# Performance work log

Measured on AMD Instinct MI355X. Metric: run time of the kernel, lower is better.

## Reference

```python
import jax, jax.numpy as jnp
import numpy as np

N_HEAD = 16
E = 1024
B, T = 2, 2048


def setup_inputs() -> dict:
    key = jax.random.key(0)
    ks = jax.random.split(key, 5)
    s = 1.0 / np.sqrt(E)
    return {
        "x": jax.random.normal(ks[0], (B, T, E), dtype=jnp.float32),
        "w_qkv": jax.random.normal(ks[1], (E, 3 * E), dtype=jnp.float32) * s,
        "b_qkv": jnp.zeros((3 * E,), dtype=jnp.float32),
        "w_proj": jax.random.normal(ks[2], (E, E), dtype=jnp.float32) * s,
        "b_proj": jnp.zeros((E,), dtype=jnp.float32),
    }


def reference(x, w_qkv, b_qkv, w_proj, b_proj):
    Bsz, Tlen, Emb = x.shape
    hd = Emb // N_HEAD
    qkv = x @ w_qkv + b_qkv  # [B, T, 3E]
    q, k, v = jnp.split(qkv, 3, axis=-1)
    # [B, H, T, hd]
    q = q.reshape(Bsz, Tlen, N_HEAD, hd).transpose(0, 2, 1, 3)
    k = k.reshape(Bsz, Tlen, N_HEAD, hd).transpose(0, 2, 1, 3)
    v = v.reshape(Bsz, Tlen, N_HEAD, hd).transpose(0, 2, 1, 3)
    scale = 1.0 / jnp.sqrt(jnp.asarray(hd, dtype=x.dtype))
    scores = jnp.einsum("bhqd,bhkd->bhqk", q, k) * scale  # [B, H, T, T]
    causal = jnp.tril(jnp.ones((Tlen, Tlen), dtype=bool))
    scores = jnp.where(causal, scores, jnp.asarray(-jnp.inf, dtype=scores.dtype))
    attn = jax.nn.softmax(scores, axis=-1)
    y = jnp.einsum("bhqk,bhkd->bhqd", attn, v)  # [B, H, T, hd]
    y = y.transpose(0, 2, 1, 3).reshape(Bsz, Tlen, Emb)
    return y @ w_proj + b_proj
```

## Files before the change

kernel.cpp:

```cpp
#include <hip/hip_runtime.h>
#include <hip/hip_bf16.h>

typedef __hip_bfloat16 bf16;
typedef __attribute__((ext_vector_type(8))) short sh8;
typedef __attribute__((ext_vector_type(4))) float f32x4;

#define BB 2
#define TT 2048
#define EE 1024
#define NH 16
#define HD 64
#define M_ROWS (BB * TT)
#define PPAD 72

__device__ __forceinline__ float b2f(bf16 v) { return __bfloat162float(v); }
__device__ __forceinline__ bf16 f2b(float v) { return __float2bfloat16(v); }
__device__ __forceinline__ unsigned short f2bu(float v) {
    union { bf16 b; unsigned short u; } x; x.b = f2b(v); return x.u;
}

__device__ __forceinline__ void gl2lds16(const bf16* g, bf16* l) {
    __builtin_amdgcn_global_load_lds(
        (__attribute__((address_space(1))) void*)g,
        (__attribute__((address_space(3))) void*)l, 16, 0, 0);
}

__global__ __launch_bounds__(256) void prep(
    const float* __restrict__ x, bf16* __restrict__ xb,
    const float* __restrict__ Wq, bf16* __restrict__ Wqt,
    const float* __restrict__ Wp, bf16* __restrict__ Wpt) {
    const int bid = blockIdx.x;
    if (bid < 4096) {
        const int i = bid * 256 + threadIdx.x;
        const float4 v = ((const float4*)x)[i];
        ushort4 u;
        u.x = f2bu(v.x); u.y = f2bu(v.y); u.z = f2bu(v.z); u.w = f2bu(v.w);
        ((ushort4*)xb)[i] = u;
        return;
    }
    __shared__ float Ld[64][65];
    const float* src; bf16* dst; int ncols, nc0, kr0;
    if (bid < 4096 + 768) {
        const int t = bid - 4096;
        src = Wq; dst = Wqt; ncols = 3072;
        nc0 = (t % 48) * 64; kr0 = (t / 48) * 64;
    } else {
        const int t = bid - 4096 - 768;
        src = Wp; dst = Wpt; ncols = 1024;
        nc0 = (t % 16) * 64; kr0 = (t / 16) * 64;
    }
#pragma unroll
    for (int i = 0; i < 16; ++i) {
        const int e = threadIdx.x + i * 256;
        Ld[e >> 6][e & 63] = src[(size_t)(kr0 + (e >> 6)) * ncols + nc0 + (e & 63)];
    }
    __syncthreads();
#pragma unroll
    for (int i = 0; i < 16; ++i) {
        const int e = threadIdx.x + i * 256;
        const int r2 = e & 63, c2 = e >> 6;
        dst[(size_t)(nc0 + c2) * EE + kr0 + r2] = f2b(Ld[r2][c2]);
    }
}

__device__ __forceinline__ void mfma_gemm_core(
    const bf16* __restrict__ A, const bf16* __restrict__ Bt,
    int m0, int n0, f32x4 acc[4][4], bf16* Al, bf16* Bl) {
    const int tid = threadIdx.x, w = tid >> 6, lane = tid & 63;
    const int li = lane & 15, quad = lane >> 4;
    const int wm = (w & 1) * 64, wn = (w >> 1) * 64;
    const int srow = w * 32 + (lane >> 3);
    const int scol = (lane & 7) * 8;

#pragma unroll
    for (int mt = 0; mt < 4; ++mt)
#pragma unroll
        for (int nt = 0; nt < 4; ++nt) acc[mt][nt] = (f32x4){0.f, 0.f, 0.f, 0.f};

    for (int k0 = 0; k0 < EE; k0 += 64) {
        __syncthreads();
#pragma unroll
        for (int j = 0; j < 4; ++j) {
            const int row = srow + j * 8;
            const int sk = scol ^ ((row & 7) * 8);
            gl2lds16(A  + (size_t)(m0 + row) * EE + k0 + sk, Al + row * 64 + scol);
            gl2lds16(Bt + (size_t)(n0 + row) * EE + k0 + sk, Bl + row * 64 + scol);
        }
        __syncthreads();
#pragma unroll
        for (int ks = 0; ks < 2; ++ks) {
            const int kof = (ks * 32 + quad * 8) ^ ((li & 7) * 8);
            sh8 af[4], bv[4];
#pragma unroll
            for (int mt = 0; mt < 4; ++mt)
                af[mt] = *(const sh8*)(Al + (wm + mt * 16 + li) * 64 + kof);
#pragma unroll
            for (int nt = 0; nt < 4; ++nt)
                bv[nt] = *(const sh8*)(Bl + (wn + nt * 16 + li) * 64 + kof);
#pragma unroll
            for (int mt = 0; mt < 4; ++mt)
#pragma unroll
                for (int nt = 0; nt < 4; ++nt)
                    acc[mt][nt] = __builtin_amdgcn_mfma_f32_16x16x32_bf16(
                        af[mt], bv[nt], acc[mt][nt], 0, 0, 0);
        }
    }
}

#define QBM 256
#define QBN 256
#define QBK 64
#define QNT (EE / QBK)

__global__ __launch_bounds__(512, 2) void gemm_qkv_8ph(
    const bf16* __restrict__ A, const bf16* __restrict__ Bt,
    const float* __restrict__ bias,
    bf16* __restrict__ Qb, bf16* __restrict__ Kb, bf16* __restrict__ Vb) {
    __shared__ bf16 Al[2][QBM * QBK];
    __shared__ bf16 Bl[2][QBN * QBK];

    const int tid  = threadIdx.x;
    const int lane = tid & 63;
    const int w    = tid >> 6;
    const int li   = lane & 15, quad = lane >> 4;
    const int wr   = w >> 2, wc = w & 3;
    const int wm   = wr << 7, wn = wc << 6;
    const int m0   = blockIdx.y << 8, n0 = blockIdx.x << 8;

    const int srow = tid >> 3;
    const int scol = (tid & 7) << 3;
    const int sg   = scol ^ ((srow & 7) << 3);
    const int swz  = (li & 7) << 3;
    const int kof0 = (quad << 3) ^ swz;
    const int kof1 = (32 + (quad << 3)) ^ swz;

    f32x4 acc[8][4];
#pragma unroll
    for (int m = 0; m < 8; ++m)
#pragma unroll
        for (int n = 0; n < 4; ++n) acc[m][n] = (f32x4){0.f, 0.f, 0.f, 0.f};

    sh8 ra[8][2];
    sh8 rb[4][2];

#define QSTAGE_A(t, h) do {                                                    \
        const int _k0 = (t) * QBK; bf16* _lb = &Al[(t) & 1][0];                \
        _Pragma("unroll")                                                      \
        for (int _j = 0; _j < 2; ++_j) {                                       \
            const int _r = ((h) << 7) + (_j << 6) + srow;                      \
            gl2lds16(A + (size_t)(m0 + _r) * EE + _k0 + sg,                    \
                     _lb + _r * QBK + scol);                                   \
        }                                                                      \
    } while (0)

#define QSTAGE_B(t, h) do {                                                    \
        const int _k0 = (t) * QBK; bf16* _lb = &Bl[(t) & 1][0];                \
        _Pragma("unroll")                                                      \
        for (int _j = 0; _j < 2; ++_j) {                                       \
            const int _r = ((h) << 7) + (_j << 6) + srow;                      \
            gl2lds16(Bt + (size_t)(n0 + _r) * EE + _k0 + sg,                   \
                     _lb + _r * QBK + scol);                                   \
        }                                                                      \
    } while (0)

#define QLOAD_A(cb, a) do {                                                    \
        const bf16* _ab = &Al[cb][0];                                          \
        _Pragma("unroll")                                                      \
        for (int _m = 0; _m < 4; ++_m) {                                       \
            const int _row = wm + (((a) << 2) + _m) * 16 + li;                 \
            ra[((a) << 2) + _m][0] = *(const sh8*)(_ab + _row * QBK + kof0);   \
            ra[((a) << 2) + _m][1] = *(const sh8*)(_ab + _row * QBK + kof1);   \
        }                                                                      \
    } while (0)

#define QLOAD_B(cb, b) do {                                                    \
        const bf16* _bb = &Bl[cb][0];                                          \
        _Pragma("unroll")                                                      \
        for (int _n = 0; _n < 2; ++_n) {                                       \
            const int _row = wn + (((b) << 1) + _n) * 16 + li;                 \
            rb[((b) << 1) + _n][0] = *(const sh8*)(_bb + _row * QBK + kof0);   \
            rb[((b) << 1) + _n][1] = *(const sh8*)(_bb + _row * QBK + kof1);   \
        }                                                                      \
    } while (0)

#define QMFMA(a, b) do {                                                       \
        _Pragma("unroll")                                                      \
        for (int _m = 0; _m < 4; ++_m)                                         \
            _Pragma("unroll")                                                  \
            for (int _n = 0; _n < 2; ++_n) {                                   \
                acc[((a) << 2) + _m][((b) << 1) + _n] =                        \
                    __builtin_amdgcn_mfma_f32_16x16x32_bf16(                   \
                        ra[((a) << 2) + _m][0], rb[((b) << 1) + _n][0],        \
                        acc[((a) << 2) + _m][((b) << 1) + _n], 0, 0, 0);       \
                acc[((a) << 2) + _m][((b) << 1) + _n] =                        \
                    __builtin_amdgcn_mfma_f32_16x16x32_bf16(                   \
                        ra[((a) << 2) + _m][1], rb[((b) << 1) + _n][1],        \
                        acc[((a) << 2) + _m][((b) << 1) + _n], 0, 0, 0);       \
            }                                                                  \
    } while (0)

#define PH_MID() do { __builtin_amdgcn_s_barrier();                            \
        asm volatile("s_waitcnt lgkmcnt(0)" ::: "memory");                     \
        __builtin_amdgcn_s_setprio(1); } while (0)
#define PH_END() do { __builtin_amdgcn_s_setprio(0);                           \
        __builtin_amdgcn_s_barrier(); } while (0)
#define PH_END_VM4() do { __builtin_amdgcn_s_setprio(0);                       \
        asm volatile("s_waitcnt vmcnt(4)" ::: "memory");                       \
        __builtin_amdgcn_s_barrier(); } while (0)

    QSTAGE_A(0, 0); QSTAGE_A(0, 1); QSTAGE_B(0, 0); QSTAGE_B(0, 1);
    QSTAGE_A(1, 0); QSTAGE_A(1, 1);
    asm volatile("s_waitcnt vmcnt(4)" ::: "memory");
    __builtin_amdgcn_s_barrier();

#pragma unroll 1
    for (int i = 0; i < QNT / 2 - 1; ++i) {
        const int t1 = 2 * i + 1, t2 = 2 * i + 2, t3 = 2 * i + 3;
        QLOAD_A(0, 0); QLOAD_B(0, 0); QSTAGE_B(t1, 0);
        PH_MID(); QMFMA(0, 0); PH_END();
        QLOAD_A(0, 1); QSTAGE_B(t1, 1);
        PH_MID(); QMFMA(1, 0); PH_END();
        QLOAD_B(0, 1); QSTAGE_A(t2, 0);
        PH_MID(); QMFMA(0, 1); PH_END();
        QSTAGE_A(t2, 1);
        PH_MID(); QMFMA(1, 1); PH_END_VM4();
        QLOAD_A(1, 0); QLOAD_B(1, 0); QSTAGE_B(t2, 0);
        PH_MID(); QMFMA(0, 0); PH_END();
        QLOAD_A(1, 1); QSTAGE_B(t2, 1);
        PH_MID(); QMFMA(1, 0); PH_END();
        QLOAD_B(1, 1); QSTAGE_A(t3, 0);
        PH_MID(); QMFMA(0, 1); PH_END();
        QSTAGE_A(t3, 1);
        PH_MID(); QMFMA(1, 1); PH_END_VM4();
    }

    QSTAGE_B(QNT - 1, 0); QSTAGE_B(QNT - 1, 1);
    QLOAD_A(0, 0); QLOAD_B(0, 0); QMFMA(0, 0);
    QLOAD_A(0, 1); QMFMA(1, 0);
    QLOAD_B(0, 1); QMFMA(0, 1); QMFMA(1, 1);
    asm volatile("s_waitcnt vmcnt(0)" ::: "memory");
    __builtin_amdgcn_s_barrier();
    QLOAD_A(1, 0); QLOAD_B(1, 0); QMFMA(0, 0);
    QLOAD_A(1, 1); QMFMA(1, 0);
    QLOAD_B(1, 1); QMFMA(0, 1); QMFMA(1, 1);

#undef QSTAGE_A
#undef QSTAGE_B
#undef QLOAD_A
#undef QLOAD_B
#undef QMFMA
#undef PH_MID
#undef PH_END
#undef PH_END_VM4

    const int which = n0 >> 10;
#pragma unroll
    for (int nt = 0; nt < 4; ++nt) {
        const int n = n0 + wn + nt * 16 + li;
        const int hseg = n & 1023;
        const int h = hseg >> 6, d = hseg & 63;
        const float bv = bias[n];
        if (which == 2) {
#pragma unroll
            for (int mt = 0; mt < 8; ++mt) {
                const int mb = m0 + wm + mt * 16 + quad * 4;
                const int b = mb >> 11, t = mb & (TT - 1);
                ushort4 u;
                u.x = f2bu(acc[mt][nt][0] + bv);
                u.y = f2bu(acc[mt][nt][1] + bv);
                u.z = f2bu(acc[mt][nt][2] + bv);
                u.w = f2bu(acc[mt][nt][3] + bv);
                *(ushort4*)(Vb + ((size_t)((b * NH + h) * HD + d)) * TT + t) = u;
            }
        } else {
            bf16* dst = (which == 0) ? Qb : Kb;
            const float scl = (which == 0) ? 0.125f : 1.0f;
#pragma unroll
            for (int mt = 0; mt < 8; ++mt)
#pragma unroll
                for (int r = 0; r < 4; ++r) {
                    const int m = m0 + wm + mt * 16 + quad * 4 + r;
                    const int b = m >> 11, t = m & (TT - 1);
                    dst[((size_t)(b * NH + h) * TT + t) * HD + d] =
                        f2b((acc[mt][nt][r] + bv) * scl);
                }
        }
    }
}

__global__ __launch_bounds__(256) void gemm_proj_mfma(
    const bf16* __restrict__ A, const bf16* __restrict__ Bt,
    const float* __restrict__ bias, float* __restrict__ C) {
    __shared__ bf16 Al[128 * 64];
    __shared__ bf16 Bl[128 * 64];
    f32x4 acc[4][4];
    const int m0 = blockIdx.y * 128, n0 = blockIdx.x * 128;
    mfma_gemm_core(A, Bt, m0, n0, acc, Al, Bl);

    const int tid = threadIdx.x, w = tid >> 6, lane = tid & 63;
    const int li = lane & 15, quad = lane >> 4;
    const int wm = (w & 1) * 64, wn = (w >> 1) * 64;

#pragma unroll
    for (int nt = 0; nt < 4; ++nt) {
        const int n = n0 + wn + nt * 16 + li;
        const float bv = bias[n];
#pragma unroll
        for (int mt = 0; mt < 4; ++mt)
#pragma unroll
            for (int r = 0; r < 4; ++r) {
                const int m = m0 + wm + mt * 16 + quad * 4 + r;
                C[(size_t)m * EE + n] = acc[mt][nt][r] + bv;
            }
    }
}

__global__ __launch_bounds__(256) void attn_mfma(
    const bf16* __restrict__ Q, const bf16* __restrict__ K,
    const bf16* __restrict__ Vt, bf16* __restrict__ Y) {
    __shared__ bf16 Kl[2][64 * 64];
    __shared__ bf16 Vl[2][64 * 64];
    __shared__ bf16 Pl[4][16 * PPAD];

    const int tid  = threadIdx.x;
    const int w    = tid >> 6;
    const int lane = tid & 63;
    const int li   = lane & 15;
    const int quad = lane >> 4;
    const int swz  = (li & 7) * 8;
    const int idx  = blockIdx.x;
    const int qb   = 31 - (idx >> 5);
    const int bh   = idx & 31;
    const int q0   = qb << 6;
    const int qw0  = q0 + w * 16;

    const bf16* Qb = Q  + (size_t)bh * TT * HD;
    const bf16* Kb = K  + (size_t)bh * TT * HD;
    const bf16* Vb = Vt + (size_t)bh * HD * TT;

    sh8 qf0 = *(const sh8*)(Qb + (size_t)(qw0 + li) * HD + quad * 8);
    sh8 qf1 = *(const sh8*)(Qb + (size_t)(qw0 + li) * HD + 32 + quad * 8);

    f32x4 o[4];
#pragma unroll
    for (int nt = 0; nt < 4; ++nt) o[nt] = (f32x4){0.f, 0.f, 0.f, 0.f};
    float lacc = 0.f;

    const int l8 = lane >> 3, l7 = lane & 7;
    const int gcol = ((l7 ^ l8) * 8);

    const int ntiles = qb + 1;
#pragma unroll
    for (int c = 0; c < 2; ++c) {
        const int rb = w * 16 + c * 8;
        gl2lds16(Kb + (size_t)(rb + l8) * HD + gcol, &Kl[0][rb * 64]);
        gl2lds16(Vb + (size_t)(rb + l8) * TT + gcol, &Vl[0][rb * 64]);
    }

    for (int it = 0; it < ntiles; ++it) {
        const int cur = it & 1;
        __syncthreads();
        if (it + 1 < ntiles) {
            const int j1 = (it + 1) << 6;
            const int nxt = cur ^ 1;
#pragma unroll
            for (int c = 0; c < 2; ++c) {
                const int rb = w * 16 + c * 8;
                gl2lds16(Kb + (size_t)(j1 + rb + l8) * HD + gcol, &Kl[nxt][rb * 64]);
                gl2lds16(Vb + (size_t)(rb + l8) * TT + j1 + gcol, &Vl[nxt][rb * 64]);
            }
        }
        const bf16* kb = &Kl[cur][0];
        const bf16* vb = &Vl[cur][0];

        const bool diag = (it == ntiles - 1);
#pragma unroll
        for (int nt = 0; nt < 4; ++nt) {
            f32x4 a = (f32x4){0.f, 0.f, 0.f, 0.f};
            sh8 kf0 = *(const sh8*)(kb + (nt * 16 + li) * 64 + ((quad * 8) ^ swz));
            a = __builtin_amdgcn_mfma_f32_16x16x32_bf16(kf0, qf0, a, 0, 0, 0);
            sh8 kf1 = *(const sh8*)(kb + (nt * 16 + li) * 64 + ((32 + quad * 8) ^ swz));
            a = __builtin_amdgcn_mfma_f32_16x16x32_bf16(kf1, qf1, a, 0, 0, 0);

            ushort4 u;
            float p0, p1, p2, p3;
            if (diag) {
                const int keyb = q0 + nt * 16 + quad * 4;
                const int qg = qw0 + li;
                p0 = (keyb + 0 > qg) ? 0.f : __expf(a[0]);
                p1 = (keyb + 1 > qg) ? 0.f : __expf(a[1]);
                p2 = (keyb + 2 > qg) ? 0.f : __expf(a[2]);
                p3 = (keyb + 3 > qg) ? 0.f : __expf(a[3]);
            } else {
                p0 = __expf(a[0]); p1 = __expf(a[1]);
                p2 = __expf(a[2]); p3 = __expf(a[3]);
            }
            lacc += (p0 + p1) + (p2 + p3);
            u.x = f2bu(p0); u.y = f2bu(p1); u.z = f2bu(p2); u.w = f2bu(p3);
            *(ushort4*)(&Pl[w][li * PPAD + nt * 16 + quad * 4]) = u;
        }

#pragma unroll
        for (int ks = 0; ks < 2; ++ks) {
            sh8 pf = *(const sh8*)(&Pl[w][li * PPAD + ks * 32 + quad * 8]);
#pragma unroll
            for (int nt = 0; nt < 4; ++nt) {
                sh8 vf = *(const sh8*)(vb + (nt * 16 + li) * 64 +
                                       ((ks * 32 + quad * 8) ^ swz));
                o[nt] = __builtin_amdgcn_mfma_f32_16x16x32_bf16(pf, vf, o[nt], 0, 0, 0);
            }
        }
    }

    lacc += __shfl_xor(lacc, 16, 64);
    lacc += __shfl_xor(lacc, 32, 64);
    float rinv[4];
#pragma unroll
    for (int r = 0; r < 4; ++r)
        rinv[r] = 1.0f / __shfl(lacc, quad * 4 + r, 64);

    const int b = bh >> 4, h = bh & 15;
#pragma unroll
    for (int nt = 0; nt < 4; ++nt)
#pragma unroll
        for (int r = 0; r < 4; ++r) {
            const int q = qw0 + quad * 4 + r;
            Y[((size_t)(b * TT + q)) * EE + h * HD + nt * 16 + li] =
                f2b(o[nt][r] * rinv[r]);
        }
}

extern "C" void kernel_launch(void* const* d_in, const int* in_sizes, int n_in,
                              void* d_out, int out_size, void* d_ws, size_t ws_size,
                              hipStream_t stream) {
    const float* x      = (const float*)d_in[0];
    const float* w_qkv  = (const float*)d_in[1];
    const float* b_qkv  = (const float*)d_in[2];
    const float* w_proj = (const float*)d_in[3];
    const float* b_proj = (const float*)d_in[4];
    float* out = (float*)d_out;

    const size_t SZ = (size_t)M_ROWS * EE;
    bf16* Q   = (bf16*)d_ws;
    bf16* K   = Q + SZ;
    bf16* V   = K + SZ;
    bf16* XB  = V + SZ;
    bf16* WQT = XB + SZ;
    bf16* WPT = WQT + 3 * SZ / 4;
    bf16* Y   = XB;

    prep<<<dim3(4096 + 768 + 256), dim3(256), 0, stream>>>(
        x, XB, w_qkv, WQT, w_proj, WPT);

    gemm_qkv_8ph<<<dim3(12, 16), dim3(512), 0, stream>>>(XB, WQT, b_qkv, Q, K, V);

    attn_mfma<<<dim3((TT / 64) * (BB * NH)), dim3(256), 0, stream>>>(Q, K, V, Y);

    gemm_proj_mfma<<<dim3(8, 32), dim3(256), 0, stream>>>(Y, WPT, b_proj, out);
}
```

Baseline: 184.5 us.

## Halve A-fragment registers by reordering MFMA quadrants in QKV GEMM pipeline

Reorders the four MFMA sub-tiles per K-step into a serpentine order (00, 01, 11, 10) so only four A fragments are live at once, and splits the B fragments into two double-buffered register sets. The global-to-LDS staging schedule is reshuffled to match, prefetching B ahead instead of A, and the epilogue is rewritten with phased barriers. The aim is to cut VGPR pressure in the 256x256-tile GEMM, which can free registers or allow better overlap. The more complex staging order risks LDS hazards or extra stalls.

```diff
diff --git a/kernel.cpp b/kernel.cpp
--- a/kernel.cpp
+++ b/kernel.cpp
@@ -140,8 +140,9 @@
 #pragma unroll
         for (int n = 0; n < 4; ++n) acc[m][n] = (f32x4){0.f, 0.f, 0.f, 0.f};
 
-    sh8 ra[8][2];
-    sh8 rb[4][2];
+    sh8 ra[4][2];
+    sh8 rb0[2][2];
+    sh8 rb1[2][2];
 
 #define QSTAGE_A(t, h) do {                                                    \
         const int _k0 = (t) * QBK; bf16* _lb = &Al[(t) & 1][0];                \
@@ -168,33 +169,33 @@
         _Pragma("unroll")                                                      \
         for (int _m = 0; _m < 4; ++_m) {                                       \
             const int _row = wm + (((a) << 2) + _m) * 16 + li;                 \
-            ra[((a) << 2) + _m][0] = *(const sh8*)(_ab + _row * QBK + kof0);   \
-            ra[((a) << 2) + _m][1] = *(const sh8*)(_ab + _row * QBK + kof1);   \
+            ra[_m][0] = *(const sh8*)(_ab + _row * QBK + kof0);                \
+            ra[_m][1] = *(const sh8*)(_ab + _row * QBK + kof1);                \
         }                                                                      \
     } while (0)
 
-#define QLOAD_B(cb, b) do {                                                    \
+#define QLOAD_B(cb, b, R) do {                                                 \
         const bf16* _bb = &Bl[cb][0];                                          \
         _Pragma("unroll")                                                      \
         for (int _n = 0; _n < 2; ++_n) {                                       \
             const int _row = wn + (((b) << 1) + _n) * 16 + li;                 \
-            rb[((b) << 1) + _n][0] = *(const sh8*)(_bb + _row * QBK + kof0);   \
-            rb[((b) << 1) + _n][1] = *(const sh8*)(_bb + _row * QBK + kof1);   \
+            R[_n][0] = *(const sh8*)(_bb + _row * QBK + kof0);                 \
+            R[_n][1] = *(const sh8*)(_bb + _row * QBK + kof1);                 \
         }                                                                      \
     } while (0)
 
-#define QMFMA(a, b) do {                                                       \
+#define QMFMA(a, b, R) do {                                                    \
         _Pragma("unroll")                                                      \
         for (int _m = 0; _m < 4; ++_m)                                         \
             _Pragma("unroll")                                                  \
             for (int _n = 0; _n < 2; ++_n) {                                   \
                 acc[((a) << 2) + _m][((b) << 1) + _n] =                        \
                     __builtin_amdgcn_mfma_f32_16x16x32_bf16(                   \
-                        ra[((a) << 2) + _m][0], rb[((b) << 1) + _n][0],        \
+                        ra[_m][0], R[_n][0],                                   \
                         acc[((a) << 2) + _m][((b) << 1) + _n], 0, 0, 0);       \
                 acc[((a) << 2) + _m][((b) << 1) + _n] =                        \
                     __builtin_amdgcn_mfma_f32_16x16x32_bf16(                   \
-                        ra[((a) << 2) + _m][1], rb[((b) << 1) + _n][1],        \
+                        ra[_m][1], R[_n][1],                                   \
                         acc[((a) << 2) + _m][((b) << 1) + _n], 0, 0, 0);       \
             }                                                                  \
     } while (0)
@@ -207,42 +208,51 @@
 #define PH_END_VM4() do { __builtin_amdgcn_s_setprio(0);                       \
         asm volatile("s_waitcnt vmcnt(4)" ::: "memory");                       \
         __builtin_amdgcn_s_barrier(); } while (0)
+#define PH_END_VM0() do { __builtin_amdgcn_s_setprio(0);                       \
+        asm volatile("s_waitcnt vmcnt(0)" ::: "memory");                       \
+        __builtin_amdgcn_s_barrier(); } while (0)
 
     QSTAGE_A(0, 0); QSTAGE_A(0, 1); QSTAGE_B(0, 0); QSTAGE_B(0, 1);
-    QSTAGE_A(1, 0); QSTAGE_A(1, 1);
+    QSTAGE_B(1, 0); QSTAGE_B(1, 1);
     asm volatile("s_waitcnt vmcnt(4)" ::: "memory");
     __builtin_amdgcn_s_barrier();
 
 #pragma unroll 1
     for (int i = 0; i < QNT / 2 - 1; ++i) {
-        const int t1 = 2 * i + 1, t2 = 2 * i + 2, t3 = 2 * i + 3;
-        QLOAD_A(0, 0); QLOAD_B(0, 0); QSTAGE_B(t1, 0);
-        PH_MID(); QMFMA(0, 0); PH_END();
-        QLOAD_A(0, 1); QSTAGE_B(t1, 1);
-        PH_MID(); QMFMA(1, 0); PH_END();
-        QLOAD_B(0, 1); QSTAGE_A(t2, 0);
-        PH_MID(); QMFMA(0, 1); PH_END();
-        QSTAGE_A(t2, 1);
-        PH_MID(); QMFMA(1, 1); PH_END_VM4();
-        QLOAD_A(1, 0); QLOAD_B(1, 0); QSTAGE_B(t2, 0);
-        PH_MID(); QMFMA(0, 0); PH_END();
-        QLOAD_A(1, 1); QSTAGE_B(t2, 1);
-        PH_MID(); QMFMA(1, 0); PH_END();
-        QLOAD_B(1, 1); QSTAGE_A(t3, 0);
-        PH_MID(); QMFMA(0, 1); PH_END();
-        QSTAGE_A(t3, 1);
-        PH_MID(); QMFMA(1, 1); PH_END_VM4();
-    }
-
-    QSTAGE_B(QNT - 1, 0); QSTAGE_B(QNT - 1, 1);
-    QLOAD_A(0, 0); QLOAD_B(0, 0); QMFMA(0, 0);
-    QLOAD_A(0, 1); QMFMA(1, 0);
-    QLOAD_B(0, 1); QMFMA(0, 1); QMFMA(1, 1);
-    asm volatile("s_waitcnt vmcnt(0)" ::: "memory");
-    __builtin_amdgcn_s_barrier();
-    QLOAD_A(1, 0); QLOAD_B(1, 0); QMFMA(0, 0);
-    QLOAD_A(1, 1); QMFMA(1, 0);
-    QLOAD_B(1, 1); QMFMA(0, 1); QMFMA(1, 1);
+        const int ta = 2 * i + 1, tb = 2 * i + 2, tc = 2 * i + 3;
+        QLOAD_A(0, 0); QLOAD_B(0, 0, rb0); QSTAGE_A(ta, 0);
+        PH_MID(); QMFMA(0, 0, rb0); PH_END();
+        QLOAD_B(0, 1, rb1); QSTAGE_A(ta, 1);
+        PH_MID(); QMFMA(0, 1, rb1); PH_END();
+        QLOAD_A(0, 1); QSTAGE_B(tb, 0);
+        PH_MID(); QMFMA(1, 1, rb1); PH_END();
+        QSTAGE_B(tb, 1);
+        PH_MID(); QMFMA(1, 0, rb0); PH_END_VM4();
+        QLOAD_A(1, 0); QLOAD_B(1, 0, rb0); QSTAGE_A(tb, 0);
+        PH_MID(); QMFMA(0, 0, rb0); PH_END();
+        QLOAD_B(1, 1, rb1); QSTAGE_A(tb, 1);
+        PH_MID(); QMFMA(0, 1, rb1); PH_END();
+        QLOAD_A(1, 1); QSTAGE_B(tc, 0);
+        PH_MID(); QMFMA(1, 1, rb1); PH_END();
+        QSTAGE_B(tc, 1);
+        PH_MID(); QMFMA(1, 0, rb0); PH_END_VM4();
+    }
+
+    QLOAD_A(0, 0); QLOAD_B(0, 0, rb0); QSTAGE_A(QNT - 1, 0);
+    PH_MID(); QMFMA(0, 0, rb0); PH_END();
+    QLOAD_B(0, 1, rb1); QSTAGE_A(QNT - 1, 1);
+    PH_MID(); QMFMA(0, 1, rb1); PH_END();
+    QLOAD_A(0, 1);
+    PH_MID(); QMFMA(1, 1, rb1); PH_END();
+    PH_MID(); QMFMA(1, 0, rb0); PH_END_VM0();
+    QLOAD_A(1, 0); QLOAD_B(1, 0, rb0);
+    PH_MID(); QMFMA(0, 0, rb0); PH_END();
+    QLOAD_B(1, 1, rb1);
+    PH_MID(); QMFMA(0, 1, rb1); PH_END();
+    QLOAD_A(1, 1);
+    PH_MID(); QMFMA(1, 1, rb1); PH_END();
+    PH_MID(); QMFMA(1, 0, rb0);
+    __builtin_amdgcn_s_setprio(0);
 
 #undef QSTAGE_A
 #undef QSTAGE_B
@@ -252,6 +262,7 @@
 #undef PH_MID
 #undef PH_END
 #undef PH_END_VM4
+#undef PH_END_VM0
 
     const int which = n0 >> 10;
 #pragma unroll
```

After: 180.7 us (median of 2 runs). 1.02x faster.
